# Optimization experiments

Measured on AMD Instinct MI355X. Metric: run time of the kernel, lower is better.

Reference implementation:

```python
import jax, jax.numpy as jnp
import numpy as np

B, N, M, K = 4, 16384, 16384, 16   # batch, points, centers, neighbors
C, O, G = 64, 64, 8                # in_planes, out_planes, group


def setup_inputs() -> dict:
    key = jax.random.key(0)
    ks = jax.random.split(key, 16)
    r = lambda i, sh, s=1.0: jax.random.normal(ks[i], sh, jnp.float32) * s
    return dict(
        center_pos=r(0, (B, M, 3)),
        center_fea=r(1, (B, C, M)),
        pos=r(2, (B, N, 3)),
        fea=r(3, (B, C, N)),
        idx=jax.random.randint(ks[4], (B, M, K), 0, N, jnp.int32),
        # linear q/k/v
        Wq=r(5, (C, O), 0.05), bq=jnp.zeros((O,), jnp.float32),
        Wk=r(6, (C, O), 0.05), bk=jnp.zeros((O,), jnp.float32),
        Wv=r(7, (C, O), 0.05), bv=jnp.zeros((O,), jnp.float32),
        # center_pos_encode: conv1x1(3->O, no bias) + folded BN (scale,shift) + relu + conv1x1(O->O)
        cpe_w1=r(8, (3, O), 0.05), cpe_s=jnp.ones((O,), jnp.float32), cpe_b=jnp.zeros((O,), jnp.float32),
        cpe_w2=r(9, (O, O), 0.05), cpe_b2=jnp.zeros((O,), jnp.float32),
        # pos_encode (Conv2d 1x1 == per-point linear)
        pe_w1=r(10, (3, O), 0.05), pe_s=jnp.ones((O,), jnp.float32), pe_b=jnp.zeros((O,), jnp.float32),
        pe_w2=r(11, (O, O), 0.05), pe_b2=jnp.zeros((O,), jnp.float32),
        # weight_encode (O -> G)
        we_w1=r(12, (O, G), 0.05), we_s=jnp.ones((G,), jnp.float32), we_b=jnp.zeros((G,), jnp.float32),
        we_w2=r(13, (G, G), 0.05), we_b2=jnp.zeros((G,), jnp.float32),
    )


def _mlp2(x, w1, s, b, w2, b2):
    # conv1x1(no bias) -> inference BatchNorm folded to (scale, shift) -> ReLU -> conv1x1(+bias)
    h = jax.nn.relu(x @ w1 * s + b)
    return h @ w2 + b2


def reference(center_pos, center_fea, pos, fea, idx,
              Wq, bq, Wk, bk, Wv, bv,
              cpe_w1, cpe_s, cpe_b, cpe_w2, cpe_b2,
              pe_w1, pe_s, pe_b, pe_w2, pe_b2,
              we_w1, we_s, we_b, we_w2, we_b2):
    x_q = center_fea.transpose(0, 2, 1) @ Wq + bq        # [B,M,O]
    ft = fea.transpose(0, 2, 1)                          # [B,N,C]
    x_k = ft @ Wk + bk                                   # [B,N,O]
    x_v = ft @ Wv + bv                                   # [B,N,O]

    gather = jax.vmap(lambda a, i: a[i])                 # per-batch irregular gather
    nk = gather(x_k, idx)                                # [B,M,K,O]
    nv = gather(x_v, idx)                                # [B,M,K,O]
    npos = gather(pos, idx) - center_pos[:, :, None, :]  # [B,M,K,3] relative coords

    cpr = _mlp2(center_pos, cpe_w1, cpe_s, cpe_b, cpe_w2, cpe_b2)  # [B,M,O]
    pr = _mlp2(npos, pe_w1, pe_s, pe_b, pe_w2, pe_b2)              # [B,M,K,O]

    r_qk = nk - x_q[:, :, None, :] + cpr[:, :, None, :]  # [B,M,K,O]
    v = nv + pr                                          # [B,M,K,O]

    w = _mlp2(r_qk, we_w1, we_s, we_b, we_w2, we_b2)     # [B,M,K,G]
    w = jax.nn.softmax(w, axis=2)                        # softmax over neighbors

    v = v.reshape(B, M, K, G, O // G)
    out = jnp.einsum('bmkgi,bmkg->bmgi', v, w).reshape(B, M, O)
    return out.transpose(0, 2, 1)                        # [B,O,M]
```

## Files before the change

kernel.cpp:

```cpp
#include <hip/hip_runtime.h>
#include <hip/hip_bf16.h>

typedef unsigned short u16;
typedef __attribute__((ext_vector_type(8))) __bf16 bf8v;
typedef __attribute__((ext_vector_type(8))) _Float16 f16x8;
typedef __attribute__((ext_vector_type(2))) _Float16 h2v;
typedef __attribute__((ext_vector_type(4))) float f32x4;
typedef __attribute__((ext_vector_type(4))) unsigned uint4v;

#define B_ 4
#define N_ 16384
#define M_ 16384
#define K_ 16
#define C_ 64
#define O_ 64
#define G_ 8

__device__ __forceinline__ float bf2f(u16 x){
  union { unsigned u; float f; } v; v.u = ((unsigned)x) << 16; return v.f;
}
__device__ __forceinline__ u16 f2bf(float f){
  union { float f; unsigned u; } v; v.f = f;
  unsigned u = v.u;
  return (u16)((u + 0x7FFFu + ((u >> 16) & 1u)) >> 16);
}
__device__ __forceinline__ u16 f2h(float f){
  union { _Float16 h; u16 u; } v; v.h = (_Float16)f; return v.u;
}
__device__ __forceinline__ h2v mkh2(float a, float b){
  h2v r = {(_Float16)a, (_Float16)b}; return r;
}

__global__ __launch_bounds__(256) void pre_kernel(
    const float* __restrict__ center_pos, const float* __restrict__ center_fea,
    const float* __restrict__ pos, const float* __restrict__ fea,
    const float* __restrict__ Wq, const float* __restrict__ bq,
    const float* __restrict__ Wk, const float* __restrict__ bk,
    const float* __restrict__ Wv, const float* __restrict__ bv,
    const float* __restrict__ cpe_w1, const float* __restrict__ cpe_s, const float* __restrict__ cpe_b,
    const float* __restrict__ cpe_w2, const float* __restrict__ cpe_b2,
    const float* __restrict__ we_w1,
    u16* __restrict__ xk, u16* __restrict__ xv, float* __restrict__ qw,
    float* __restrict__ pos4, float* __restrict__ cp4)
{
  __shared__ u16 sWT[128*72];
  __shared__ u16 sA[64*72];
  __shared__ u16 sOut[64*136];
  __shared__ float sMisc[256];
  __shared__ float sCi[8];
  int tid = threadIdx.x;
  int l = tid & 63, w = tid >> 6, c = l & 15, q = l >> 4;
  int blk = blockIdx.x;

  if (blk < 256){
    int P0 = blk * 256; int b = P0 >> 14; int n00 = P0 & (N_-1);
    const float* fb = fea + (long)b*C_*N_;
    for (int e = tid; e < 8192; e += 256){
      int k = e >> 7, col = e & 127;
      float v = (col < 64) ? Wk[k*64 + col] : Wv[k*64 + (col-64)];
      sWT[col*72 + k] = f2bf(v);
    }
    if (tid < 128) sMisc[tid] = (tid < 64) ? bk[tid] : bv[tid-64];
    {
      long pg = (long)P0 + tid;
      f32x4 r = {pos[pg*3], pos[pg*3+1], pos[pg*3+2], 0.f};
      ((f32x4*)pos4)[pg] = r;
    }

    #pragma unroll 1
    for (int s = 0; s < 4; s++){
      int n0 = n00 + s*64;
      #pragma unroll
      for (int pp = 0; pp < 4; pp++){
        int k = pp*16 + (tid >> 4);
        int nf = (tid & 15)*4;
        f32x4 v = *(const f32x4*)&fb[(long)k*N_ + n0 + nf];
        sA[(nf+0)*72+k] = f2bf(v[0]); sA[(nf+1)*72+k] = f2bf(v[1]);
        sA[(nf+2)*72+k] = f2bf(v[2]); sA[(nf+3)*72+k] = f2bf(v[3]);
      }
      __syncthreads();

      bf8v af0 = *(const bf8v*)&sA[(w*16+c)*72 + q*8];
      bf8v af1 = *(const bf8v*)&sA[(w*16+c)*72 + 32 + q*8];
      f32x4 acc[8];
      #pragma unroll
      for (int t = 0; t < 8; t++){
        float bb = sMisc[16*t + c];
        f32x4 a_ = {bb, bb, bb, bb};
        bf8v b0 = *(const bf8v*)&sWT[(16*t + c)*72 + q*8];
        bf8v b1 = *(const bf8v*)&sWT[(16*t + c)*72 + 32 + q*8];
        a_ = __builtin_amdgcn_mfma_f32_16x16x32_bf16(af0, b0, a_, 0,0,0);
        a_ = __builtin_amdgcn_mfma_f32_16x16x32_bf16(af1, b1, a_, 0,0,0);
        acc[t] = a_;
      }
      #pragma unroll
      for (int t = 0; t < 8; t++)
        #pragma unroll
        for (int r = 0; r < 4; r++)
          sOut[(w*16 + q*4 + r)*136 + 16*t + c] = f2bf(acc[t][r]);
      __syncthreads();

      #pragma unroll
      for (int rep = 0; rep < 4; rep++){
        int chunk = rep*256 + tid;
        int pt = chunk >> 4, c8i = chunk & 15;
        uint4v val = *(const uint4v*)&sOut[pt*136 + c8i*8];
        int col8 = c8i*8;
        long row = (long)P0 + s*64 + pt;
        if (col8 < 64) *(uint4v*)(xk + row*64 + col8)      = val;
        else           *(uint4v*)(xv + row*64 + (col8-64)) = val;
      }
      __syncthreads();
    }
  } else {
    int P0 = (blk - 256) * 256; int b = P0 >> 14; int m00 = P0 & (M_-1);
    const float* cfb = center_fea + (long)b*C_*M_;
    float* sWe = (float*)sOut;
    float* sQ  = (float*)sOut;
    for (int e = tid; e < 512; e += 256) sWe[e] = we_w1[e];
    if (tid < 64){
      float sc = cpe_s[tid];
      sMisc[tid]     = cpe_w1[tid]*sc;
      sMisc[64+tid]  = cpe_w1[64+tid]*sc;
      sMisc[128+tid] = cpe_w1[128+tid]*sc;
      sMisc[192+tid] = cpe_b[tid];
    }
    {
      long pg = (long)P0 + tid;
      f32x4 r = {center_pos[pg*3], center_pos[pg*3+1], center_pos[pg*3+2], 0.f};
      ((f32x4*)cp4)[pg] = r;
    }
    __syncthreads();
    {
      int k = tid >> 1, g0 = (tid & 1)*4;
      const float* brow = (k < 64) ? (cpe_w2 + k*64) : (Wq + (k-64)*64);
      float sgn = (k < 64) ? 1.f : -1.f;
      float aw[4] = {0.f,0.f,0.f,0.f};
      for (int o = 0; o < 64; o++){
        float bo = brow[o]*sgn;
        #pragma unroll
        for (int gg=0; gg<4; gg++) aw[gg] += bo * sWe[o*8 + g0+gg];
      }
      #pragma unroll
      for (int gg=0; gg<4; gg++) sWT[(g0+gg)*136 + k] = f2bf(aw[gg]);
    }
    for (int e = tid; e < 2176; e += 256){
      int r = e / 136, cc = e % 136;
      if (r >= 8 || cc >= 128) sWT[e] = 0;
    }
    if (tid < 8){
      float s = 0.f;
      for (int o = 0; o < 64; o++) s += (cpe_b2[o] - bq[o]) * sWe[o*8 + tid];
      sCi[tid] = s;
    }
    __syncthreads();

    #pragma unroll 1
    for (int s = 0; s < 4; s++){
      int m0 = m00 + s*64;
      #pragma unroll
      for (int pp = 0; pp < 4; pp++){
        int k = pp*16 + (tid >> 4);
        int nf = (tid & 15)*4;
        f32x4 v = *(const f32x4*)&cfb[(long)k*M_ + m0 + nf];
        sA[(nf+0)*72+k] = f2bf(v[0]); sA[(nf+1)*72+k] = f2bf(v[1]);
        sA[(nf+2)*72+k] = f2bf(v[2]); sA[(nf+3)*72+k] = f2bf(v[3]);
      }
      long c3 = (long)(P0 + s*64 + w*16 + c)*3;
      float cp0 = center_pos[c3], cp1 = center_pos[c3+1], cp2 = center_pos[c3+2];
      __syncthreads();

      bf8v ah[2];
      #pragma unroll
      for (int ks = 0; ks < 2; ks++){
        union { bf8v v; u16 sv[8]; } ua;
        #pragma unroll
        for (int j = 0; j < 8; j++){
          int h = ks*32 + q*8 + j;
          float hv = cp0*sMisc[h] + cp1*sMisc[64+h] + cp2*sMisc[128+h] + sMisc[192+h];
          ua.sv[j] = f2bf(fmaxf(hv, 0.f));
        }
        ah[ks] = ua.v;
      }
      bf8v acf0 = *(const bf8v*)&sA[(w*16+c)*72 + q*8];
      bf8v acf1 = *(const bf8v*)&sA[(w*16+c)*72 + 32 + q*8];

      float ci = (c < 8) ? sCi[c] : 0.f;
      f32x4 aq = {ci, ci, ci, ci};
      {
        bf8v b0 = *(const bf8v*)&sWT[c*136 + q*8];
        bf8v b1 = *(const bf8v*)&sWT[c*136 + 32 + q*8];
        bf8v b2 = *(const bf8v*)&sWT[c*136 + 64 + q*8];
        bf8v b3 = *(const bf8v*)&sWT[c*136 + 96 + q*8];
        aq = __builtin_amdgcn_mfma_f32_16x16x32_bf16(ah[0], b0, aq, 0,0,0);
        aq = __builtin_amdgcn_mfma_f32_16x16x32_bf16(ah[1], b1, aq, 0,0,0);
        aq = __builtin_amdgcn_mfma_f32_16x16x32_bf16(acf0,  b2, aq, 0,0,0);
        aq = __builtin_amdgcn_mfma_f32_16x16x32_bf16(acf1,  b3, aq, 0,0,0);
      }
      __syncthreads();
      if (c < 8){
        #pragma unroll
        for (int r = 0; r < 4; r++) sQ[(w*16 + q*4 + r)*8 + c] = aq[r];
      }
      __syncthreads();
      for (int e = tid; e < 512; e += 256)
        qw[(long)(P0 + s*64)*8 + e] = sQ[e];
      __syncthreads();
    }
  }
}

__global__ __launch_bounds__(256) void attn_kernel(
    const float* __restrict__ cp4, const float* __restrict__ pos4,
    const int* __restrict__ idx,
    const float* __restrict__ pe_w1, const float* __restrict__ pe_s, const float* __restrict__ pe_b,
    const float* __restrict__ pe_w2, const float* __restrict__ pe_b2,
    const float* __restrict__ we_w1, const float* __restrict__ we_s, const float* __restrict__ we_b,
    const float* __restrict__ we_w2, const float* __restrict__ we_b2,
    const u16* __restrict__ xk, const u16* __restrict__ xv, const float* __restrict__ qw,
    float* __restrict__ out)
{
  int tid = threadIdx.x;
  __shared__ float s_w1f[192], s_pb[64], s_pb2[64], s_ww2[64];
  __shared__ float s_ws8[8], s_wb8[8], s_wb28[8];
  __shared__ f32x4 s_dyn4[1312];
  __shared__ float s_tile[32*66];

  char* dynb = (char*)s_dyn4;

  if (tid < 64){
    float sc = pe_s[tid];
    s_w1f[tid]     = pe_w1[tid]*sc;
    s_w1f[64+tid]  = pe_w1[64+tid]*sc;
    s_w1f[128+tid] = pe_w1[128+tid]*sc;
    s_pb[tid]  = pe_b[tid];
    s_pb2[tid] = pe_b2[tid];
    s_ww2[tid] = we_w2[tid];
  }
  if (tid >= 64 && tid < 72){
    int g = tid-64;
    s_ws8[g]=we_s[g]; s_wb8[g]=we_b[g]; s_wb28[g]=we_b2[g];
  }
  u16* stg = (u16*)dynb;
  #pragma unroll
  for (int pp = 0; pp < 4; pp++){
    int row = pp*16 + (tid >> 4);
    int colf = (tid & 15)*4;
    f32x4 v = *(const f32x4*)&pe_w2[row*64 + colf];
    stg[(colf+0)*72+row] = f2h(v[0]); stg[(colf+1)*72+row] = f2h(v[1]);
    stg[(colf+2)*72+row] = f2h(v[2]); stg[(colf+3)*72+row] = f2h(v[3]);
  }
  u16* stg2 = (u16*)(dynb + 9216);
  for (int e = tid; e < 512; e += 256){
    int k = e >> 3, cc = e & 7;
    stg2[cc*72 + k] = f2bf(we_w1[e]);
  }
  for (int e = tid; e < 576; e += 256) stg2[576 + e] = 0;
  __syncthreads();

  int w = tid >> 6, l = tid & 63, c = l & 15, q = l >> 4, c8 = c & 7;

  f16x8 pw2f[4][2];
  bf8v ww1f[2];
  f16x8 w2B, hz8;
  #pragma unroll
  for (int t = 0; t < 4; t++){
    pw2f[t][0] = *(const f16x8*)&stg[(t*16+c)*72 + q*8];
    pw2f[t][1] = *(const f16x8*)&stg[(t*16+c)*72 + 32 + q*8];
  }
  ww1f[0] = *(const bf8v*)&stg2[c*72 + q*8];
  ww1f[1] = *(const bf8v*)&stg2[c*72 + 32 + q*8];
  {
    union { f16x8 v; u16 s[8]; } uu;
    #pragma unroll
    for (int j = 0; j < 8; j++)
      uu.s[j] = (q == 0 && c < 8) ? f2h(s_ww2[j*8 + c]) : (u16)0;
    w2B = uu.v;
    #pragma unroll
    for (int j = 0; j < 8; j++) uu.s[j] = 0;
    hz8 = uu.v;
  }
  h2v cw0[2][4], cw1[2][4], cw2[2][4], cb[2][4];
  #pragma unroll
  for (int ks = 0; ks < 2; ks++)
    #pragma unroll
    for (int jj = 0; jj < 4; jj++){
      int o = ks*32 + q*8 + jj*2;
      cw0[ks][jj] = mkh2(s_w1f[o],     s_w1f[o+1]);
      cw1[ks][jj] = mkh2(s_w1f[64+o],  s_w1f[65+o]);
      cw2[ks][jj] = mkh2(s_w1f[128+o], s_w1f[129+o]);
      cb [ks][jj] = mkh2(s_pb[o],      s_pb[o+1]);
    }
  float ws_c = s_ws8[c8], wb_c = s_wb8[c8], wb2_c = s_wb28[c8];
  float pb2l = s_pb2[l];
  h2v hz2 = {(_Float16)0.f, (_Float16)0.f};
  __syncthreads();

  float* sv  = (float*)(dynb + w*5248);
  float* swt = (float*)(dynb + w*5248 + 4352);
  u16*  sh   = (u16*) (dynb + w*5248 + 4992);

  int blk = blockIdx.x;
  int pbase = (((blk & 7) << 8) | (blk >> 3)) * 32;
  int b = pbase >> 14;
  const u16* xkb = xk + (long)b * N_ * 64;
  const u16* xvb = xv + (long)b * N_ * 64;
  const f32x4* pos4b = ((const f32x4*)pos4) + (long)b * N_;
  int ch = c >> 3;
  int gl = l >> 3;

  int pb0 = pbase + w*8;
  const int*   idxl = idx + (long)pb0*16 + c;
  const float* qwl  = qw  + (long)pb0*8 + c8;
  const f32x4* cp4l = ((const f32x4*)cp4) + pb0;

  int iv0 = idxl[0];
  int ivt = idxl[16];
  int iv2 = idxl[32];
  float q0 = qwl[0], q1 = qwl[8], q2 = qwl[16];
  f32x4 cpv = cp4l[0];
  f32x4 ppA = pos4b[iv0];
  const u16* krA = xkb + (size_t)iv0*64;
  bf8v kaA0 = *(const bf8v*)(krA + q*8);
  bf8v kaA1 = *(const bf8v*)(krA + 32 + q*8);
  const u16* vrA = xvb + (size_t)iv0*64;
  uint4v vaA0 = *(const uint4v*)(vrA + q*8);
  uint4v vaA1 = *(const uint4v*)(vrA + 32 + q*8);
  f32x4 ppB = pos4b[ivt];
  const u16* krB = xkb + (size_t)ivt*64;
  bf8v kaB0 = *(const bf8v*)(krB + q*8);
  bf8v kaB1 = *(const bf8v*)(krB + 32 + q*8);
  const u16* vrB = xvb + (size_t)ivt*64;
  uint4v vaB0 = *(const uint4v*)(vrB + q*8);
  uint4v vaB1 = *(const uint4v*)(vrB + 32 + q*8);

  #pragma unroll 1
  for (int i = 0; i < 8; i++){
    f32x4 ppN = pos4b[iv2];
    const u16* krN = xkb + (size_t)iv2*64;
    bf8v kaN0 = *(const bf8v*)(krN + q*8);
    bf8v kaN1 = *(const bf8v*)(krN + 32 + q*8);
    const u16* vrN = xvb + (size_t)iv2*64;
    uint4v vaN0 = *(const uint4v*)(vrN + q*8);
    uint4v vaN1 = *(const uint4v*)(vrN + 32 + q*8);
    int ni = (i < 7) ? i+1 : 7;
    f32x4 cpn = cp4l[ni];
    int n3 = (i < 5) ? i+3 : 7;
    int iv3 = idxl[n3*16];
    float q3 = qwl[n3*8];

    {
      unsigned a0 = vaA0[0], a1 = vaA0[1], a2 = vaA0[2], a3 = vaA0[3];
      f32x4 lo0 = {bf2f((u16)a0), bf2f((u16)(a0>>16)), bf2f((u16)a1), bf2f((u16)(a1>>16))};
      f32x4 hi0 = {bf2f((u16)a2), bf2f((u16)(a2>>16)), bf2f((u16)a3), bf2f((u16)(a3>>16))};
      unsigned b0 = vaA1[0], b1 = vaA1[1], b2 = vaA1[2], b3 = vaA1[3];
      f32x4 lo1 = {bf2f((u16)b0), bf2f((u16)(b0>>16)), bf2f((u16)b1), bf2f((u16)(b1>>16))};
      f32x4 hi1 = {bf2f((u16)b2), bf2f((u16)(b2>>16)), bf2f((u16)b3), bf2f((u16)(b3>>16))};
      f32x4* d0 = (f32x4*)&sv[c*68 + q*8];
      d0[0] = lo0; d0[1] = hi0;
      f32x4* d1 = (f32x4*)&sv[c*68 + 32 + q*8];
      d1[0] = lo1; d1[1] = hi1;
    }

    float np0 = ppA[0] - cpv[0], np1 = ppA[1] - cpv[1], np2 = ppA[2] - cpv[2];
    h2v np0h = {(_Float16)np0, (_Float16)np0};
    h2v np1h = {(_Float16)np1, (_Float16)np1};
    h2v np2h = {(_Float16)np2, (_Float16)np2};
    f16x8 h1f[2];
    #pragma unroll
    for (int ks = 0; ks < 2; ks++){
      union { f16x8 v; h2v p[4]; } hu;
      #pragma unroll
      for (int jj = 0; jj < 4; jj++){
        h2v a = cb[ks][jj];
        a = np0h*cw0[ks][jj] + a;
        a = np1h*cw1[ks][jj] + a;
        a = np2h*cw2[ks][jj] + a;
        hu.p[jj] = __builtin_elementwise_max(a, hz2);
      }
      h1f[ks] = hu.v;
    }

    f32x4 h2a = {q0, q0, q0, q0};
    h2a = __builtin_amdgcn_mfma_f32_16x16x32_bf16(kaA0, ww1f[0], h2a, 0,0,0);
    h2a = __builtin_amdgcn_mfma_f32_16x16x32_bf16(kaA1, ww1f[1], h2a, 0,0,0);

    if (c < 8){
      #pragma unroll
      for (int r = 0; r < 4; r++)
        sh[(q*4+r)*8 + c] = f2h(fmaxf(h2a[r]*ws_c + wb_c, 0.f));
    }
    f16x8 hrow = *(const f16x8*)&sh[c*8];
    f16x8 ahf = (q == 0) ? hrow : hz8;

    f32x4 wlv = {wb2_c, wb2_c, wb2_c, wb2_c};
    wlv = __builtin_amdgcn_mfma_f32_16x16x32_f16(ahf, w2B, wlv, 0,0,0);

    float e0 = exp2f(wlv[0]*1.44269504f);
    float e1 = exp2f(wlv[1]*1.44269504f);
    float e2 = exp2f(wlv[2]*1.44269504f);
    float e3 = exp2f(wlv[3]*1.44269504f);
    float sm = e0+e1+e2+e3;
    sm += __shfl_xor(sm, 16, 64);
    sm += __shfl_xor(sm, 32, 64);
    float rn = 1.0f / sm;
    if (c < 8){
      f32x4 ev = {e0*rn, e1*rn, e2*rn, e3*rn};
      *(f32x4*)&swt[c*20 + q*4] = ev;
    }

    float ov[4];
    #pragma unroll
    for (int t = 0; t < 4; t++){
      f32x4 z = {0.f,0.f,0.f,0.f};
      z = __builtin_amdgcn_mfma_f32_16x16x32_f16(h1f[0], pw2f[t][0], z, 0,0,0);
      z = __builtin_amdgcn_mfma_f32_16x16x32_f16(h1f[1], pw2f[t][1], z, 0,0,0);
      f32x4 wv = *(const f32x4*)&swt[(t*2+ch)*20 + q*4];
      ov[t] = z[0]*wv[0] + z[1]*wv[1] + z[2]*wv[2] + z[3]*wv[3];
    }
    #pragma unroll
    for (int t = 0; t < 4; t++){
      ov[t] += __shfl_xor(ov[t], 16, 64);
      ov[t] += __shfl_xor(ov[t], 32, 64);
    }
    float ovsel = ov[0];
    ovsel = (q==1) ? ov[1] : ovsel;
    ovsel = (q==2) ? ov[2] : ovsel;
    ovsel = (q==3) ? ov[3] : ovsel;

    float vacc = 0.f;
    {
      const f32x4* wr4 = (const f32x4*)&swt[gl*20];
      const float* svl = &sv[l];
      #pragma unroll
      for (int k4 = 0; k4 < 4; k4++){
        f32x4 wv = wr4[k4];
        vacc += svl[(4*k4+0)*68]*wv[0];
        vacc += svl[(4*k4+1)*68]*wv[1];
        vacc += svl[(4*k4+2)*68]*wv[2];
        vacc += svl[(4*k4+3)*68]*wv[3];
      }
    }

    s_tile[(w*8+i)*66 + l] = ovsel + vacc + pb2l;

    kaA0 = kaB0; kaA1 = kaB1; vaA0 = vaB0; vaA1 = vaB1; ppA = ppB;
    kaB0 = kaN0; kaB1 = kaN1; vaB0 = vaN0; vaB1 = vaN1; ppB = ppN;
    cpv = cpn;
    iv2 = iv3; q0 = q1; q1 = q2; q2 = q3;
  }
  __syncthreads();

  int o0 = tid >> 5, pt = tid & 31;
  int m0 = pbase & (M_-1);
  long outb = ((long)b*64) * M_ + m0 + pt;
  #pragma unroll
  for (int ii = 0; ii < 8; ii++){
    int o = o0*8 + ii;
    out[outb + (long)o*M_] = s_tile[pt*66 + o];
  }
}

extern "C" void kernel_launch(void* const* d_in, const int* in_sizes, int n_in,
                              void* d_out, int out_size, void* d_ws, size_t ws_size,
                              hipStream_t stream) {
  const float* center_pos = (const float*)d_in[0];
  const float* center_fea = (const float*)d_in[1];
  const float* pos        = (const float*)d_in[2];
  const float* fea        = (const float*)d_in[3];
  const int*   idx        = (const int*)d_in[4];
  const float* Wq = (const float*)d_in[5];   const float* bq = (const float*)d_in[6];
  const float* Wk = (const float*)d_in[7];   const float* bk = (const float*)d_in[8];
  const float* Wv = (const float*)d_in[9];   const float* bv = (const float*)d_in[10];
  const float* cpe_w1 = (const float*)d_in[11]; const float* cpe_s = (const float*)d_in[12];
  const float* cpe_b  = (const float*)d_in[13]; const float* cpe_w2 = (const float*)d_in[14];
  const float* cpe_b2 = (const float*)d_in[15];
  const float* pe_w1 = (const float*)d_in[16]; const float* pe_s = (const float*)d_in[17];
  const float* pe_b  = (const float*)d_in[18]; const float* pe_w2 = (const float*)d_in[19];
  const float* pe_b2 = (const float*)d_in[20];
  const float* we_w1 = (const float*)d_in[21]; const float* we_s = (const float*)d_in[22];
  const float* we_b  = (const float*)d_in[23]; const float* we_w2 = (const float*)d_in[24];
  const float* we_b2 = (const float*)d_in[25];

  const size_t SZ = (size_t)B_*N_*64;
  u16* xk = (u16*)d_ws;
  u16* xv = xk + SZ;
  float* qwp = (float*)(xv + SZ);
  float* pos4p = qwp + (size_t)B_*M_*8;
  float* cp4p  = pos4p + (size_t)B_*N_*4;
  float* outp = (float*)d_out;

  hipLaunchKernelGGL(pre_kernel, dim3(512), dim3(256), 0, stream,
      center_pos, center_fea, pos, fea, Wq, bq, Wk, bk, Wv, bv,
      cpe_w1, cpe_s, cpe_b, cpe_w2, cpe_b2, we_w1,
      xk, xv, qwp, pos4p, cp4p);
  hipLaunchKernelGGL(attn_kernel, dim3(2048), dim3(256), 0, stream,
      cp4p, pos4p, idx, pe_w1, pe_s, pe_b, pe_w2, pe_b2,
      we_w1, we_s, we_b, we_w2, we_b2, xk, xv, qwp, outp);
}
```

Before: 204.8 us.

## Shrink pre_kernel tiles to 64 points per block and quadruple grid

Each pre_kernel block now handles a single 64-point tile instead of looping over four, and the grid grows from 512 to 2048 blocks. This exposes more parallelism, and the sOut buffer is aliased onto sWT to cut LDS use so more blocks can be resident per CU. Weight loads are vectorized and the center-feature load is hoisted before the weight-folding step so the two overlap. The cost is that weight staging and the qw weight folding are now redone four times as often across blocks.

```diff
diff --git a/kernel.cpp b/kernel.cpp
--- a/kernel.cpp
+++ b/kernel.cpp
@@ -45,78 +45,78 @@
 {
   __shared__ u16 sWT[128*72];
   __shared__ u16 sA[64*72];
-  __shared__ u16 sOut[64*136];
   __shared__ float sMisc[256];
   __shared__ float sCi[8];
   int tid = threadIdx.x;
   int l = tid & 63, w = tid >> 6, c = l & 15, q = l >> 4;
   int blk = blockIdx.x;
 
-  if (blk < 256){
-    int P0 = blk * 256; int b = P0 >> 14; int n00 = P0 & (N_-1);
+  if (blk < 1024){
+    int P0 = blk * 64; int b = P0 >> 14; int n0 = P0 & (N_-1);
     const float* fb = fea + (long)b*C_*N_;
-    for (int e = tid; e < 8192; e += 256){
-      int k = e >> 7, col = e & 127;
-      float v = (col < 64) ? Wk[k*64 + col] : Wv[k*64 + (col-64)];
-      sWT[col*72 + k] = f2bf(v);
+    int g4 = (tid & 31) * 4;
+    const float* wbase = (g4 < 64) ? (Wk + g4) : (Wv + g4 - 64);
+    #pragma unroll
+    for (int it = 0; it < 8; it++){
+      int k = it*8 + (tid >> 5);
+      f32x4 v = *(const f32x4*)&wbase[k*64];
+      sWT[(g4+0)*72+k] = f2bf(v[0]); sWT[(g4+1)*72+k] = f2bf(v[1]);
+      sWT[(g4+2)*72+k] = f2bf(v[2]); sWT[(g4+3)*72+k] = f2bf(v[3]);
     }
     if (tid < 128) sMisc[tid] = (tid < 64) ? bk[tid] : bv[tid-64];
-    {
+    if (tid < 64){
       long pg = (long)P0 + tid;
       f32x4 r = {pos[pg*3], pos[pg*3+1], pos[pg*3+2], 0.f};
       ((f32x4*)pos4)[pg] = r;
     }
-
-    #pragma unroll 1
-    for (int s = 0; s < 4; s++){
-      int n0 = n00 + s*64;
+    #pragma unroll
+    for (int pp = 0; pp < 4; pp++){
+      int k = pp*16 + (tid >> 4);
+      int nf = (tid & 15)*4;
+      f32x4 v = *(const f32x4*)&fb[(long)k*N_ + n0 + nf];
+      sA[(nf+0)*72+k] = f2bf(v[0]); sA[(nf+1)*72+k] = f2bf(v[1]);
+      sA[(nf+2)*72+k] = f2bf(v[2]); sA[(nf+3)*72+k] = f2bf(v[3]);
+    }
+    __syncthreads();
+
+    bf8v af0 = *(const bf8v*)&sA[(w*16+c)*72 + q*8];
+    bf8v af1 = *(const bf8v*)&sA[(w*16+c)*72 + 32 + q*8];
+    f32x4 acc[8];
+    #pragma unroll
+    for (int t = 0; t < 8; t++){
+      float bb = sMisc[16*t + c];
+      f32x4 a_ = {bb, bb, bb, bb};
+      bf8v b0 = *(const bf8v*)&sWT[(16*t + c)*72 + q*8];
+      bf8v b1 = *(const bf8v*)&sWT[(16*t + c)*72 + 32 + q*8];
+      a_ = __builtin_amdgcn_mfma_f32_16x16x32_bf16(af0, b0, a_, 0,0,0);
+      a_ = __builtin_amdgcn_mfma_f32_16x16x32_bf16(af1, b1, a_, 0,0,0);
+      acc[t] = a_;
+    }
+    __syncthreads();
+
+    u16* sOut = sWT;
+    #pragma unroll
+    for (int t = 0; t < 8; t++)
       #pragma unroll
-      for (int pp = 0; pp < 4; pp++){
-        int k = pp*16 + (tid >> 4);
-        int nf = (tid & 15)*4;
-        f32x4 v = *(const f32x4*)&fb[(long)k*N_ + n0 + nf];
-        sA[(nf+0)*72+k] = f2bf(v[0]); sA[(nf+1)*72+k] = f2bf(v[1]);
-        sA[(nf+2)*72+k] = f2bf(v[2]); sA[(nf+3)*72+k] = f2bf(v[3]);
-      }
-      __syncthreads();
-
-      bf8v af0 = *(const bf8v*)&sA[(w*16+c)*72 + q*8];
-      bf8v af1 = *(const bf8v*)&sA[(w*16+c)*72 + 32 + q*8];
-      f32x4 acc[8];
-      #pragma unroll
-      for (int t = 0; t < 8; t++){
-        float bb = sMisc[16*t + c];
-        f32x4 a_ = {bb, bb, bb, bb};
-        bf8v b0 = *(const bf8v*)&sWT[(16*t + c)*72 + q*8];
-        bf8v b1 = *(const bf8v*)&sWT[(16*t + c)*72 + 32 + q*8];
-        a_ = __builtin_amdgcn_mfma_f32_16x16x32_bf16(af0, b0, a_, 0,0,0);
-        a_ = __builtin_amdgcn_mfma_f32_16x16x32_bf16(af1, b1, a_, 0,0,0);
-        acc[t] = a_;
-      }
-      #pragma unroll
-      for (int t = 0; t < 8; t++)
-        #pragma unroll
-        for (int r = 0; r < 4; r++)
-          sOut[(w*16 + q*4 + r)*136 + 16*t + c] = f2bf(acc[t][r]);
-      __syncthreads();
-
-      #pragma unroll
-      for (int rep = 0; rep < 4; rep++){
-        int chunk = rep*256 + tid;
-        int pt = chunk >> 4, c8i = chunk & 15;
-        uint4v val = *(const uint4v*)&sOut[pt*136 + c8i*8];
-        int col8 = c8i*8;
-        long row = (long)P0 + s*64 + pt;
-        if (col8 < 64) *(uint4v*)(xk + row*64 + col8)      = val;
-        else           *(uint4v*)(xv + row*64 + (col8-64)) = val;
-      }
-      __syncthreads();
+      for (int r = 0; r < 4; r++)
+        sOut[(w*16 + q*4 + r)*136 + 16*t + c] = f2bf(acc[t][r]);
+    __syncthreads();
+
+    #pragma unroll
+    for (int rep = 0; rep < 4; rep++){
+      int chunk = rep*256 + tid;
+      int pt = chunk >> 4, c8i = chunk & 15;
+      uint4v val = *(const uint4v*)&sOut[pt*136 + c8i*8];
+      int col8 = c8i*8;
+      long row = (long)P0 + pt;
+      if (col8 < 64) *(uint4v*)(xk + row*64 + col8)      = val;
+      else           *(uint4v*)(xv + row*64 + (col8-64)) = val;
     }
   } else {
-    int P0 = (blk - 256) * 256; int b = P0 >> 14; int m00 = P0 & (M_-1);
+    int P0 = (blk - 1024) * 64; int b = P0 >> 14; int m0 = P0 & (M_-1);
     const float* cfb = center_fea + (long)b*C_*M_;
-    float* sWe = (float*)sOut;
-    float* sQ  = (float*)sOut;
+    float* sWe = (float*)((char*)sWT + 8192);
+    float* sQ  = (float*)((char*)sWT + 12288);
     for (int e = tid; e < 512; e += 256) sWe[e] = we_w1[e];
     if (tid < 64){
       float sc = cpe_s[tid];
@@ -125,24 +125,43 @@
       sMisc[128+tid] = cpe_w1[128+tid]*sc;
       sMisc[192+tid] = cpe_b[tid];
     }
-    {
+    if (tid < 64){
       long pg = (long)P0 + tid;
       f32x4 r = {center_pos[pg*3], center_pos[pg*3+1], center_pos[pg*3+2], 0.f};
       ((f32x4*)cp4)[pg] = r;
     }
+    #pragma unroll
+    for (int pp = 0; pp < 4; pp++){
+      int k = pp*16 + (tid >> 4);
+      int nf = (tid & 15)*4;
+      f32x4 v = *(const f32x4*)&cfb[(long)k*M_ + m0 + nf];
+      sA[(nf+0)*72+k] = f2bf(v[0]); sA[(nf+1)*72+k] = f2bf(v[1]);
+      sA[(nf+2)*72+k] = f2bf(v[2]); sA[(nf+3)*72+k] = f2bf(v[3]);
+    }
     __syncthreads();
+
     {
       int k = tid >> 1, g0 = (tid & 1)*4;
       const float* brow = (k < 64) ? (cpe_w2 + k*64) : (Wq + (k-64)*64);
       float sgn = (k < 64) ? 1.f : -1.f;
-      float aw[4] = {0.f,0.f,0.f,0.f};
-      for (int o = 0; o < 64; o++){
-        float bo = brow[o]*sgn;
+      float aw0=0.f, aw1=0.f, aw2=0.f, aw3=0.f;
+      #pragma unroll 4
+      for (int o4 = 0; o4 < 16; o4++){
+        f32x4 bo4 = *(const f32x4*)&brow[o4*4];
         #pragma unroll
-        for (int gg=0; gg<4; gg++) aw[gg] += bo * sWe[o*8 + g0+gg];
+        for (int oo = 0; oo < 4; oo++){
+          float bo = bo4[oo]*sgn;
+          int o = o4*4 + oo;
+          aw0 += bo * sWe[o*8 + g0+0];
+          aw1 += bo * sWe[o*8 + g0+1];
+          aw2 += bo * sWe[o*8 + g0+2];
+          aw3 += bo * sWe[o*8 + g0+3];
+        }
       }
-      #pragma unroll
-      for (int gg=0; gg<4; gg++) sWT[(g0+gg)*136 + k] = f2bf(aw[gg]);
+      sWT[(g0+0)*136 + k] = f2bf(aw0);
+      sWT[(g0+1)*136 + k] = f2bf(aw1);
+      sWT[(g0+2)*136 + k] = f2bf(aw2);
+      sWT[(g0+3)*136 + k] = f2bf(aw3);
     }
     for (int e = tid; e < 2176; e += 256){
       int r = e / 136, cc = e % 136;
@@ -150,63 +169,49 @@
     }
     if (tid < 8){
       float s = 0.f;
+      #pragma unroll 4
       for (int o = 0; o < 64; o++) s += (cpe_b2[o] - bq[o]) * sWe[o*8 + tid];
       sCi[tid] = s;
     }
     __syncthreads();
 
-    #pragma unroll 1
-    for (int s = 0; s < 4; s++){
-      int m0 = m00 + s*64;
+    long c3 = (long)(P0 + w*16 + c)*3;
+    float cp0 = center_pos[c3], cp1 = center_pos[c3+1], cp2 = center_pos[c3+2];
+
+    bf8v ah[2];
+    #pragma unroll
+    for (int ks = 0; ks < 2; ks++){
+      union { bf8v v; u16 sv[8]; } ua;
       #pragma unroll
-      for (int pp = 0; pp < 4; pp++){
-        int k = pp*16 + (tid >> 4);
-        int nf = (tid & 15)*4;
-        f32x4 v = *(const f32x4*)&cfb[(long)k*M_ + m0 + nf];
-        sA[(nf+0)*72+k] = f2bf(v[0]); sA[(nf+1)*72+k] = f2bf(v[1]);
-        sA[(nf+2)*72+k] = f2bf(v[2]); sA[(nf+3)*72+k] = f2bf(v[3]);
+      for (int j = 0; j < 8; j++){
+        int h = ks*32 + q*8 + j;
+        float hv = cp0*sMisc[h] + cp1*sMisc[64+h] + cp2*sMisc[128+h] + sMisc[192+h];
+        ua.sv[j] = f2bf(fmaxf(hv, 0.f));
       }
-      long c3 = (long)(P0 + s*64 + w*16 + c)*3;
-      float cp0 = center_pos[c3], cp1 = center_pos[c3+1], cp2 = center_pos[c3+2];
-      __syncthreads();
-
-      bf8v ah[2];
+      ah[ks] = ua.v;
+    }
+    bf8v acf0 = *(const bf8v*)&sA[(w*16+c)*72 + q*8];
+    bf8v acf1 = *(const bf8v*)&sA[(w*16+c)*72 + 32 + q*8];
+
+    float ci = (c < 8) ? sCi[c] : 0.f;
+    f32x4 aq = {ci, ci, ci, ci};
+    {
+      bf8v b0 = *(const bf8v*)&sWT[c*136 + q*8];
+      bf8v b1 = *(const bf8v*)&sWT[c*136 + 32 + q*8];
+      bf8v b2 = *(const bf8v*)&sWT[c*136 + 64 + q*8];
+      bf8v b3 = *(const bf8v*)&sWT[c*136 + 96 + q*8];
+      aq = __builtin_amdgcn_mfma_f32_16x16x32_bf16(ah[0], b0, aq, 0,0,0);
+      aq = __builtin_amdgcn_mfma_f32_16x16x32_bf16(ah[1], b1, aq, 0,0,0);
+      aq = __builtin_amdgcn_mfma_f32_16x16x32_bf16(acf0,  b2, aq, 0,0,0);
+      aq = __builtin_amdgcn_mfma_f32_16x16x32_bf16(acf1,  b3, aq, 0,0,0);
+    }
+    if (c < 8){
       #pragma unroll
-      for (int ks = 0; ks < 2; ks++){
-        union { bf8v v; u16 sv[8]; } ua;
-        #pragma unroll
-        for (int j = 0; j < 8; j++){
-          int h = ks*32 + q*8 + j;
-          float hv = cp0*sMisc[h] + cp1*sMisc[64+h] + cp2*sMisc[128+h] + sMisc[192+h];
-          ua.sv[j] = f2bf(fmaxf(hv, 0.f));
-        }
-        ah[ks] = ua.v;
-      }
-      bf8v acf0 = *(const bf8v*)&sA[(w*16+c)*72 + q*8];
-      bf8v acf1 = *(const bf8v*)&sA[(w*16+c)*72 + 32 + q*8];
-
-      float ci = (c < 8) ? sCi[c] : 0.f;
-      f32x4 aq = {ci, ci, ci, ci};
-      {
-        bf8v b0 = *(const bf8v*)&sWT[c*136 + q*8];
-        bf8v b1 = *(const bf8v*)&sWT[c*136 + 32 + q*8];
-        bf8v b2 = *(const bf8v*)&sWT[c*136 + 64 + q*8];
-        bf8v b3 = *(const bf8v*)&sWT[c*136 + 96 + q*8];
-        aq = __builtin_amdgcn_mfma_f32_16x16x32_bf16(ah[0], b0, aq, 0,0,0);
-        aq = __builtin_amdgcn_mfma_f32_16x16x32_bf16(ah[1], b1, aq, 0,0,0);
-        aq = __builtin_amdgcn_mfma_f32_16x16x32_bf16(acf0,  b2, aq, 0,0,0);
-        aq = __builtin_amdgcn_mfma_f32_16x16x32_bf16(acf1,  b3, aq, 0,0,0);
-      }
-      __syncthreads();
-      if (c < 8){
-        #pragma unroll
-        for (int r = 0; r < 4; r++) sQ[(w*16 + q*4 + r)*8 + c] = aq[r];
-      }
-      __syncthreads();
-      for (int e = tid; e < 512; e += 256)
-        qw[(long)(P0 + s*64)*8 + e] = sQ[e];
-      __syncthreads();
-    }
+      for (int r = 0; r < 4; r++) sQ[(w*16 + q*4 + r)*8 + c] = aq[r];
+    }
+    __syncthreads();
+    for (int e = tid; e < 512; e += 256)
+      qw[(long)P0*8 + e] = sQ[e];
   }
 }
 
@@ -490,7 +495,7 @@
   float* cp4p  = pos4p + (size_t)B_*N_*4;
   float* outp = (float*)d_out;
 
-  hipLaunchKernelGGL(pre_kernel, dim3(512), dim3(256), 0, stream,
+  hipLaunchKernelGGL(pre_kernel, dim3(2048), dim3(256), 0, stream,
       center_pos, center_fea, pos, fea, Wq, bq, Wk, bk, Wv, bv,
       cpe_w1, cpe_s, cpe_b, cpe_w2, cpe_b2, we_w1,
       xk, xv, qwp, pos4p, cp4p);
```

Result: slower. 212.2 us (+3.6%).
